# Kernel optimization log

Hardware: AMD Instinct MI355X
Metric: run time of the kernel (lower is better)

The kernel has to match this reference:

```python
import jax, jax.numpy as jnp
import numpy as np
from jax import lax

LRELU_SLOPE = 0.2
GAIN = 2.0 ** 0.5
EPS = 1e-8


def setup_inputs() -> dict:
    key = jax.random.key(0)
    ks = jax.random.split(key, 8)
    B, NDW, CIN, COUT, H, W = 4, 512, 16, 16, 1024, 1024
    return {
        "w": jax.random.normal(ks[0], (B, NDW), jnp.float32),
        "x": jax.random.normal(ks[1], (B, CIN, H, W), jnp.float32),
        "noise": jax.random.normal(ks[2], (B, 1, H, W), jnp.float32),
        "fc_weight": jax.random.normal(ks[3], (CIN, NDW), jnp.float32),
        "fc_bias": jnp.ones((CIN,), jnp.float32),
        "conv_weight": jax.random.normal(ks[4], (COUT, CIN, 3, 3), jnp.float32),
        "conv_bias": jax.random.normal(ks[5], (COUT,), jnp.float32),
        "scale_noise": jnp.float32(0.1),
    }


def reference(w, x, noise, fc_weight, fc_bias, conv_weight, conv_bias, scale_noise):
    NDW = fc_weight.shape[1]
    COUT, CIN, KH, KW = conv_weight.shape
    # equal_lr scaling (FC): weight * n_dim_in**-0.5
    s = w @ (fc_weight.T * (NDW ** -0.5)) + fc_bias  # [B, CIN] style per input channel
    # equal_lr scaling (Conv): weight * (in_channels * k^2)**-0.5
    wc = conv_weight * ((CIN * KH * KW) ** -0.5)  # [COUT, CIN, 3, 3]
    # demodulation coefficient: d[b,o] = 1/sqrt(sum_{i,kh,kw} (s[b,i]*wc[o,i,kh,kw])^2 + eps)
    w2 = (wc ** 2).sum(axis=(2, 3))  # [COUT, CIN]
    d = lax.rsqrt((s ** 2) @ w2.T + EPS)  # [B, COUT]
    # modulate input instead of materializing per-sample weights (mathematically identical)
    xm = x * s[:, :, None, None]
    y = lax.conv_general_dilated(
        xm, wc, window_strides=(1, 1), padding=((1, 1), (1, 1)),
        dimension_numbers=("NCHW", "OIHW", "NCHW"))
    y = y * d[:, :, None, None] + conv_bias[None, :, None, None]
    y = y + scale_noise * noise  # broadcast noise over channels
    y = GAIN * jnp.where(y >= 0, y, LRELU_SLOPE * y)
    return (w, y)
```

## Files before the change

kernel.cpp:

```cpp
#include <hip/hip_runtime.h>

#define H_ 1024
#define W_ 1024
#define B_ 4
#define CIN 16
#define COUT 16
#define TH 8
#define TW 64
#define NT 4
#define ROWS 10
#define COLS 66

#define LRELU 0.2f
#define GAIN_ 1.4142135623730951f
#define EPS_ 1e-8f

typedef __attribute__((ext_vector_type(8))) short bf16x8;
typedef __attribute__((ext_vector_type(4))) float f32x4;

static __device__ __forceinline__ unsigned short f32_to_bf16(float f) {
    unsigned int u = __float_as_uint(f);
    unsigned int r = u + 0x7FFF + ((u >> 16) & 1);
    return (unsigned short)(r >> 16);
}

static __device__ __forceinline__ float f4c(const float4& v, int px) {
    return px == 0 ? v.x : px == 1 ? v.y : px == 2 ? v.z : v.w;
}

__global__ __launch_bounds__(256) void k_setup1(
    const float* __restrict__ w, const float* __restrict__ fcw,
    const float* __restrict__ fcb, float* __restrict__ s_out,
    float* __restrict__ w_copy_out)
{
    __shared__ float part[256];
    const int tid = threadIdx.x;
    const int bi = tid >> 2;
    const int q  = tid & 3;
    const int b = bi >> 4, i = bi & 15;
    const float* wr = w + b * 512 + q * 128;
    const float* fr = fcw + i * 512 + q * 128;
    float acc = 0.f;
    #pragma unroll 8
    for (int k = 0; k < 128; ++k) acc += wr[k] * fr[k];
    part[tid] = acc;
    __syncthreads();
    if (tid < 64) {
        float v = part[tid*4] + part[tid*4+1] + part[tid*4+2] + part[tid*4+3];
        s_out[tid] = v * 0.04419417382415922f  + fcb[tid & 15];
    }
    for (int e = tid; e < B_ * 512; e += 256) w_copy_out[e] = w[e];
}

__global__ __launch_bounds__(256) void k_setup2(
    const float* __restrict__ s_in, const float* __restrict__ convw,
    unsigned short* __restrict__ afrag)
{
    const int b = blockIdx.x;
    const int tid = threadIdx.x;
    __shared__ float s_sh[16];
    __shared__ float d_sh[16];
    __shared__ float wc_sh[COUT * CIN * 9];
    __shared__ float part[256];

    if (tid < 16) s_sh[tid] = s_in[b * 16 + tid];
    for (int e = tid; e < COUT * CIN * 9; e += 256)
        wc_sh[e] = convw[e] * (1.0f / 12.0f);
    __syncthreads();

    const int o = tid >> 4, i = tid & 15;
    const float si = s_sh[i];
    float acc = 0.f;
    #pragma unroll
    for (int tap = 0; tap < 9; ++tap) {
        float v = wc_sh[(o * 16 + i) * 9 + tap] * si;
        acc += v * v;
    }
    part[tid] = acc;
    __syncthreads();
    if (tid < 16) {
        float sum = EPS_;
        #pragma unroll
        for (int j = 0; j < 16; ++j) sum += part[tid * 16 + j];
        d_sh[tid] = rsqrtf(sum);
    }
    __syncthreads();

    for (int e = tid; e < 5 * 64 * 8; e += 256) {
        int t = e >> 9;
        int lane = (e >> 3) & 63;
        int j = e & 7;
        int oo = lane & 15, g = lane >> 4;
        int ii = (g & 1) * 8 + j;
        int tap = 2 * t + (g >> 1);
        float v = 0.f;
        if (tap < 9) v = wc_sh[(oo * 16 + ii) * 9 + tap] * s_sh[ii] * d_sh[oo];
        afrag[(size_t)b * (5 * 64 * 8) + e] = f32_to_bf16(v);
    }
}

__global__ __launch_bounds__(256, 3) void k_conv(
    const float* __restrict__ x, const float* __restrict__ noise,
    const float* __restrict__ conv_bias, const float* __restrict__ sn_ptr,
    const unsigned short* __restrict__ afrag, float* __restrict__ y)
{
    __shared__ unsigned short tile[2][2][ROWS][COLS][8];

    const int tid = threadIdx.x;
    const int bt = blockIdx.z;
    const int h0 = blockIdx.y * (TH * NT);
    const int w0 = blockIdx.x * TW;
    const float sn = sn_ptr[0];
    const float* xb = x + (size_t)bt * CIN * H_ * W_;
    float* yb = y + (size_t)bt * COUT * H_ * W_;
    const float* nb = noise + (size_t)bt * H_ * W_;

    const int lane  = tid & 63;
    const int wid   = tid >> 6;
    const int p     = lane & 15;
    const int g     = lane >> 4;
    const int ghalf = g >> 1;
    const int chalf = g & 1;

    const int rowA = tid >> 5, subA = tid & 31, hhA = subA >> 4, cgA = subA & 15;
    const int rowB = 8 + (tid >> 5);
    const bool hasB = (tid < 64);
    const bool hasE = (tid >= 64) && (tid < 104);
    const int e_  = tid - 64;
    const int rowE = e_ >> 2, sideE = (e_ >> 1) & 1, hhE = e_ & 1;

    float4 vA[8], vB[8];
    float  ev[8];

    auto stage_load = [&](int t) {
        const int gh0 = h0 + TH * t - 1;
        {
            const int gh = gh0 + rowA;
            const bool ok = (gh >= 0) && (gh < H_);
            const float* base = xb + ((size_t)(8 * hhA) * H_ + gh) * W_ + (w0 + 4 * cgA);
            #pragma unroll
            for (int c = 0; c < 8; ++c) {
                vA[c] = make_float4(0.f, 0.f, 0.f, 0.f);
                if (ok) vA[c] = *reinterpret_cast<const float4*>(base + (size_t)c * H_ * W_);
            }
        }
        if (hasB) {
            const int gh = gh0 + rowB;
            const bool ok = (gh >= 0) && (gh < H_);
            const float* base = xb + ((size_t)(8 * hhA) * H_ + gh) * W_ + (w0 + 4 * cgA);
            #pragma unroll
            for (int c = 0; c < 8; ++c) {
                vB[c] = make_float4(0.f, 0.f, 0.f, 0.f);
                if (ok) vB[c] = *reinterpret_cast<const float4*>(base + (size_t)c * H_ * W_);
            }
        } else if (hasE) {
            const int gh = gh0 + rowE;
            const int gw = w0 - 1 + sideE * (COLS - 1);
            const bool ok = (gh >= 0) && (gh < H_) && (gw >= 0) && (gw < W_);
            #pragma unroll
            for (int c = 0; c < 8; ++c)
                ev[c] = ok ? xb[((size_t)(8 * hhE + c) * H_ + gh) * W_ + gw] : 0.f;
        }
    };

    auto stage_write = [&](int buf) {
        #pragma unroll
        for (int px = 0; px < 4; ++px) {
            bf16x8 pk;
            #pragma unroll
            for (int c = 0; c < 8; ++c) pk[c] = (short)f32_to_bf16(f4c(vA[c], px));
            *reinterpret_cast<bf16x8*>(&tile[buf][hhA][rowA][1 + 4 * cgA + px][0]) = pk;
        }
        if (hasB) {
            #pragma unroll
            for (int px = 0; px < 4; ++px) {
                bf16x8 pk;
                #pragma unroll
                for (int c = 0; c < 8; ++c) pk[c] = (short)f32_to_bf16(f4c(vB[c], px));
                *reinterpret_cast<bf16x8*>(&tile[buf][hhA][rowB][1 + 4 * cgA + px][0]) = pk;
            }
        } else if (hasE) {
            bf16x8 pk;
            #pragma unroll
            for (int c = 0; c < 8; ++c) pk[c] = (short)f32_to_bf16(ev[c]);
            *reinterpret_cast<bf16x8*>(&tile[buf][hhE][rowE][sideE * (COLS - 1)][0]) = pk;
        }
    };

    bf16x8 a[5];
    {
        const bf16x8* ap = reinterpret_cast<const bf16x8*>(afrag + (size_t)bt * 5 * 64 * 8);
        #pragma unroll
        for (int t = 0; t < 5; ++t) a[t] = ap[t * 64 + lane];
    }
    float bias_j[4];
    #pragma unroll
    for (int j = 0; j < 4; ++j) bias_j[j] = conv_bias[g * 4 + j];

    int lroff[5], lcoff[5];
    #pragma unroll
    for (int t = 0; t < 5; ++t) {
        int tap = 2 * t + ghalf;
        if (tap > 8) tap = 8;
        lroff[t] = tap / 3;
        lcoff[t] = tap % 3;
    }

    auto compute = [&](int t, int buf) {
        #pragma unroll
        for (int rr = 0; rr < 2; ++rr) {
            const int oh = wid * 2 + rr;
            #pragma unroll
            for (int gc = 0; gc < 4; ++gc) {
                const int ow = gc * 16;
                f32x4 acc = {0.f, 0.f, 0.f, 0.f};
                #pragma unroll
                for (int tt = 0; tt < 5; ++tt) {
                    const bf16x8 bv = *reinterpret_cast<const bf16x8*>(
                        &tile[buf][chalf][oh + lroff[tt]][ow + p + lcoff[tt]][0]);
                    acc = __builtin_amdgcn_mfma_f32_16x16x32_bf16(a[tt], bv, acc, 0, 0, 0);
                }
                const int gh = h0 + TH * t + oh;
                const int gw = w0 + ow + p;
                const float noi = nb[(size_t)gh * W_ + gw] * sn;
                #pragma unroll
                for (int j = 0; j < 4; ++j) {
                    float vv = acc[j] + bias_j[j] + noi;
                    vv = (vv >= 0.f) ? vv : (LRELU * vv);
                    yb[((size_t)(g * 4 + j) * H_ + gh) * W_ + gw] = vv * GAIN_;
                }
            }
        }
    };

    stage_load(0);
    stage_write(0);
    for (int t = 0; t < NT - 1; ++t) {
        __syncthreads();
        stage_load(t + 1);
        compute(t, t & 1);
        stage_write((t + 1) & 1);
    }
    __syncthreads();
    compute(NT - 1, (NT - 1) & 1);
}

extern "C" void kernel_launch(void* const* d_in, const int* in_sizes, int n_in,
                              void* d_out, int out_size, void* d_ws, size_t ws_size,
                              hipStream_t stream)
{
    const float* w     = (const float*)d_in[0];
    const float* x     = (const float*)d_in[1];
    const float* noise = (const float*)d_in[2];
    const float* fcw   = (const float*)d_in[3];
    const float* fcb   = (const float*)d_in[4];
    const float* convw = (const float*)d_in[5];
    const float* convb = (const float*)d_in[6];
    const float* sn    = (const float*)d_in[7];

    float* out = (float*)d_out;
    float* ws_s = (float*)d_ws;
    unsigned short* ws_afrag = (unsigned short*)((char*)d_ws + 256);

    k_setup1<<<1, 256, 0, stream>>>(w, fcw, fcb, ws_s, out);
    k_setup2<<<B_, 256, 0, stream>>>(ws_s, convw, ws_afrag);
    dim3 grid(W_ / TW, H_ / (TH * NT), B_);
    k_conv<<<grid, 256, 0, stream>>>(x, noise, convb, sn, ws_afrag, out + 2048);
}
```

Before: 197.5 us.

## Single-buffer LDS tile, double rows per block, drop min-blocks launch bound

The conv kernel now uses one shared-memory tile instead of two, halving its LDS footprint. Each block covers twice as many row strips, and the minimum-blocks-per-SM hint is removed from the launch bounds. Register prefetch of the next strip still overlaps with the MFMA compute, but each iteration now needs an extra barrier before overwriting the tile. The aim is higher occupancy and less per-block halo and setup overhead, at the cost of more syncs and fewer blocks in the grid.

```diff
diff --git a/kernel.cpp b/kernel.cpp
--- a/kernel.cpp
+++ b/kernel.cpp
@@ -7,7 +7,7 @@
 #define COUT 16
 #define TH 8
 #define TW 64
-#define NT 4
+#define NT 8
 #define ROWS 10
 #define COLS 66
 
@@ -99,16 +99,16 @@
     }
 }
 
-__global__ __launch_bounds__(256, 3) void k_conv(
+__global__ __launch_bounds__(256) void k_conv(
     const float* __restrict__ x, const float* __restrict__ noise,
     const float* __restrict__ conv_bias, const float* __restrict__ sn_ptr,
     const unsigned short* __restrict__ afrag, float* __restrict__ y)
 {
-    __shared__ unsigned short tile[2][2][ROWS][COLS][8];
+    __shared__ unsigned short tile[2][ROWS][COLS][8];
 
     const int tid = threadIdx.x;
     const int bt = blockIdx.z;
-    const int h0 = blockIdx.y * (TH * NT);
+    const int h0s = blockIdx.y * (TH * NT);
     const int w0 = blockIdx.x * TW;
     const float sn = sn_ptr[0];
     const float* xb = x + (size_t)bt * CIN * H_ * W_;
@@ -133,7 +133,7 @@
     float  ev[8];
 
     auto stage_load = [&](int t) {
-        const int gh0 = h0 + TH * t - 1;
+        const int gh0 = h0s + TH * t - 1;
         {
             const int gh = gh0 + rowA;
             const bool ok = (gh >= 0) && (gh < H_);
@@ -163,13 +163,13 @@
         }
     };
 
-    auto stage_write = [&](int buf) {
+    auto stage_write = [&]() {
         #pragma unroll
         for (int px = 0; px < 4; ++px) {
             bf16x8 pk;
             #pragma unroll
             for (int c = 0; c < 8; ++c) pk[c] = (short)f32_to_bf16(f4c(vA[c], px));
-            *reinterpret_cast<bf16x8*>(&tile[buf][hhA][rowA][1 + 4 * cgA + px][0]) = pk;
+            *reinterpret_cast<bf16x8*>(&tile[hhA][rowA][1 + 4 * cgA + px][0]) = pk;
         }
         if (hasB) {
             #pragma unroll
@@ -177,13 +177,13 @@
                 bf16x8 pk;
                 #pragma unroll
                 for (int c = 0; c < 8; ++c) pk[c] = (short)f32_to_bf16(f4c(vB[c], px));
-                *reinterpret_cast<bf16x8*>(&tile[buf][hhA][rowB][1 + 4 * cgA + px][0]) = pk;
+                *reinterpret_cast<bf16x8*>(&tile[hhA][rowB][1 + 4 * cgA + px][0]) = pk;
             }
         } else if (hasE) {
             bf16x8 pk;
             #pragma unroll
             for (int c = 0; c < 8; ++c) pk[c] = (short)f32_to_bf16(ev[c]);
-            *reinterpret_cast<bf16x8*>(&tile[buf][hhE][rowE][sideE * (COLS - 1)][0]) = pk;
+            *reinterpret_cast<bf16x8*>(&tile[hhE][rowE][sideE * (COLS - 1)][0]) = pk;
         }
     };
 
@@ -206,10 +206,11 @@
         lcoff[t] = tap % 3;
     }
 
-    auto compute = [&](int t, int buf) {
+    auto compute = [&](int t) {
         #pragma unroll
         for (int rr = 0; rr < 2; ++rr) {
             const int oh = wid * 2 + rr;
+            const int gh = h0s + TH * t + oh;
             #pragma unroll
             for (int gc = 0; gc < 4; ++gc) {
                 const int ow = gc * 16;
@@ -217,10 +218,9 @@
                 #pragma unroll
                 for (int tt = 0; tt < 5; ++tt) {
                     const bf16x8 bv = *reinterpret_cast<const bf16x8*>(
-                        &tile[buf][chalf][oh + lroff[tt]][ow + p + lcoff[tt]][0]);
+                        &tile[chalf][oh + lroff[tt]][ow + p + lcoff[tt]][0]);
                     acc = __builtin_amdgcn_mfma_f32_16x16x32_bf16(a[tt], bv, acc, 0, 0, 0);
                 }
-                const int gh = h0 + TH * t + oh;
                 const int gw = w0 + ow + p;
                 const float noi = nb[(size_t)gh * W_ + gw] * sn;
                 #pragma unroll
@@ -234,15 +234,13 @@
     };
 
     stage_load(0);
-    stage_write(0);
-    for (int t = 0; t < NT - 1; ++t) {
+    for (int t = 0; t < NT; ++t) {
+        if (t > 0) __syncthreads();
+        stage_write();
         __syncthreads();
-        stage_load(t + 1);
-        compute(t, t & 1);
-        stage_write((t + 1) & 1);
-    }
-    __syncthreads();
-    compute(NT - 1, (NT - 1) & 1);
+        if (t + 1 < NT) stage_load(t + 1);
+        compute(t);
+    }
 }
 
 extern "C" void kernel_launch(void* const* d_in, const int* in_sizes, int n_in,
```

Result: faster. 173.0 us (-12.4%).
